# Optimization experiments

Measured on AMD Instinct MI355X. Metric: run time of the kernel, lower is better.

The kernel has to match this reference:

```python
import jax, jax.numpy as jnp
import numpy as np

B, N, C = 8, 4096, 512
H = W = 64           # N = H * W, dimensionality == 2
SHIFT = 4            # shift_size
WS = 8               # window_size
R = 4                # mlp_ratio
EPS = 1e-6


def setup_inputs() -> dict:
    key = jax.random.key(0)
    ks = jax.random.split(key, 3)
    return {
        "inputs": jax.random.normal(ks[0], (B, N, C), dtype=jnp.float32),
        # second_norm (LayerNormalization) params
        "ln_gamma": jnp.ones((C,), jnp.float32),
        "ln_beta": jnp.zeros((C,), jnp.float32),
        # MLP params: Dense(C*R) -> gelu -> Dense(C)
        "W1": jax.random.normal(ks[1], (C, C * R), dtype=jnp.float32) * 0.02,
        "b1": jnp.zeros((C * R,), jnp.float32),
        "W2": jax.random.normal(ks[2], (C * R, C), dtype=jnp.float32) * 0.02,
        "b2": jnp.zeros((C,), jnp.float32),
    }


def _layer_norm(x, gamma, beta):
    mu = jnp.mean(x, axis=-1, keepdims=True)
    var = jnp.mean(jnp.square(x - mu), axis=-1, keepdims=True)
    return (x - mu) * jax.lax.rsqrt(var + EPS) * gamma + beta


def reference(inputs, ln_gamma, ln_beta, W1, b1, W2, b2):
    # NOTE: faithful to the provided call(): first_norm and attention are
    # never invoked (`normed = x`, `self_att = windowed`), so the window
    # partition + reverse is an exact identity round-trip of the shifted grid.
    grid = inputs.reshape(B, H, W, C)
    shifted = jnp.roll(grid, (-SHIFT, -SHIFT), axis=(1, 2))  # SwinCyclicShifter

    # window partition: [B, nH, nW, WS, WS, C] windows of WSxWS patches
    nh = H // WS
    win = shifted.reshape(B, nh, WS, nh, WS, C).transpose(0, 1, 3, 2, 4, 5)
    # (identity "attention" on [B*nH*nW, WS*WS, C]) then window reverse
    unwin = win.transpose(0, 1, 3, 2, 4, 5).reshape(B, N, C)

    x = unwin + inputs                       # residual add
    normed = _layer_norm(x, ln_gamma, ln_beta)
    h = jax.nn.gelu(normed @ W1 + b1)        # [B, N, 4C]
    mlp_out = h @ W2 + b2                    # [B, N, C]
    return mlp_out + x
```

## Files before the change

### kernel.cpp

```cpp
#include <hip/hip_runtime.h>
#include <hip/hip_bf16.h>
#include <cstdint>
#include <cstddef>


typedef short bf16x8 __attribute__((ext_vector_type(8)));
typedef float f32x4 __attribute__((ext_vector_type(4)));

#define GLOBAL_AS(p) ((__attribute__((address_space(1))) void*)(uintptr_t)(p))
#define LDS_AS(p)    ((__attribute__((address_space(3))) void*)(p))

static __device__ __forceinline__ ushort f2bf(float f) {
    uint32_t u = __float_as_uint(f);
    uint32_t r = (u + 0x7FFFu + ((u >> 16) & 1u)) >> 16;
    return (ushort)r;
}

static __device__ __forceinline__ float gelu_s(float v) {
    float v2 = v * v;
    float m = fmaf(0.07135481283f, v2, 1.5957691216f);
    float e = __expf(-v * m);
    return v * __builtin_amdgcn_rcpf(1.0f + e);
}

static __device__ __forceinline__ int rolled_row(int row) {
    int b = row >> 12, n = row & 4095;
    int h = n >> 6, wv = n & 63;
    int n2 = (((h + 4) & 63) << 6) | ((wv + 4) & 63);
    return (b << 12) | n2;
}

#define SBAR() do { __builtin_amdgcn_sched_barrier(0); \
                    __builtin_amdgcn_s_barrier(); \
                    __builtin_amdgcn_sched_barrier(0); } while (0)

__global__ __launch_bounds__(128)
void ln_kernel(const float* __restrict__ in, const float* __restrict__ gamma,
               const float* __restrict__ beta, ushort* __restrict__ normed) {
    const int row = blockIdx.x;
    const int t = threadIdx.x;
    const int row2 = rolled_row(row);

    const float4* p0 = (const float4*)(in + (size_t)row * 512);
    const float4* p1 = (const float4*)(in + (size_t)row2 * 512);
    float4 a = p0[t], c = p1[t];
    float x0 = a.x + c.x, x1 = a.y + c.y, x2 = a.z + c.z, x3 = a.w + c.w;

    float s = x0 + x1 + x2 + x3;
    float sq = x0 * x0 + x1 * x1 + x2 * x2 + x3 * x3;
#pragma unroll
    for (int o = 32; o > 0; o >>= 1) {
        s += __shfl_xor(s, o);
        sq += __shfl_xor(sq, o);
    }
    __shared__ float red[4];
    if ((t & 63) == 0) { red[(t >> 6) * 2] = s; red[(t >> 6) * 2 + 1] = sq; }
    __syncthreads();
    s = red[0] + red[2];
    sq = red[1] + red[3];
    float mu = s * (1.0f / 512.0f);
    float var = sq * (1.0f / 512.0f) - mu * mu;
    float rs = rsqrtf(var + 1e-6f);

    float4 g = ((const float4*)gamma)[t];
    float4 be = ((const float4*)beta)[t];
    ushort4 o4;
    o4.x = f2bf((x0 - mu) * rs * g.x + be.x);
    o4.y = f2bf((x1 - mu) * rs * g.y + be.y);
    o4.z = f2bf((x2 - mu) * rs * g.z + be.z);
    o4.w = f2bf((x3 - mu) * rs * g.w + be.w);
    ((ushort4*)(normed + (size_t)row * 512))[t] = o4;
}

template <int PERM>
__global__ __launch_bounds__(256)
void transpose_cast(const float* __restrict__ src, ushort* __restrict__ dst,
                    int R, int Ccols) {
    __shared__ float tile[32][33];
    const int bx = blockIdx.x * 32;
    const int by = blockIdx.y * 32;
    const int tx = threadIdx.x, ty = threadIdx.y;
#pragma unroll
    for (int i = 0; i < 32; i += 8)
        tile[ty + i][tx] = src[(size_t)(by + ty + i) * Ccols + bx + tx];
    __syncthreads();
    int k = by + tx;
    int kd = PERM ? ((k & ~63) | ((k & 15) << 2) | ((k >> 4) & 3)) : k;
#pragma unroll
    for (int i = 0; i < 32; i += 8)
        dst[(size_t)(bx + ty + i) * R + kd] = f2bf(tile[tx][ty + i]);
}

__global__ __launch_bounds__(256)
void mlp_gemm1(const ushort* __restrict__ A, const ushort* __restrict__ Bt,
               const float* __restrict__ bias, ushort* __restrict__ outH) {
    constexpr int K = 512, N = 2048, BK = 32;
    __shared__ ushort Asm[128 * BK];
    __shared__ ushort Bsm[128 * BK];

    const int t = threadIdx.x;
    const int w = t >> 6, l = t & 63;
    const int wr = w >> 1, wc = w & 1;
    const int brow = blockIdx.y * 128;
    const int bcol = blockIdx.x * 128;

    f32x4 acc[4][4] = {};

    const int arow = t >> 2;
    const int acol = (t & 3) * 8;
    const size_t aBase = (size_t)(brow + arow) * K + acol;
    const size_t bBase = (size_t)(bcol + arow) * K + acol;
    char* ldsA = (char*)Asm + w * 1024;
    char* ldsB = (char*)Bsm + w * 1024;

    const int kb = (l >> 4) * 8;
    const int rA = l & 15;

    for (int k0 = 0; k0 < K; k0 += BK) {
        __builtin_amdgcn_global_load_lds(GLOBAL_AS(A + aBase + k0), LDS_AS(ldsA), 16, 0, 0);
        __builtin_amdgcn_global_load_lds(GLOBAL_AS(A + aBase + (size_t)64 * K + k0), LDS_AS(ldsA + 4096), 16, 0, 0);
        __builtin_amdgcn_global_load_lds(GLOBAL_AS(Bt + bBase + k0), LDS_AS(ldsB), 16, 0, 0);
        __builtin_amdgcn_global_load_lds(GLOBAL_AS(Bt + bBase + (size_t)64 * K + k0), LDS_AS(ldsB + 4096), 16, 0, 0);
        __syncthreads();

        bf16x8 aF[4], bF[4];
#pragma unroll
        for (int i = 0; i < 4; ++i)
            aF[i] = *(const bf16x8*)&Asm[(wr * 64 + i * 16 + rA) * BK + kb];
#pragma unroll
        for (int j = 0; j < 4; ++j)
            bF[j] = *(const bf16x8*)&Bsm[(wc * 64 + j * 16 + rA) * BK + kb];

#pragma unroll
        for (int i = 0; i < 4; ++i)
#pragma unroll
            for (int j = 0; j < 4; ++j)
                acc[i][j] = __builtin_amdgcn_mfma_f32_16x16x32_bf16(aF[i], bF[j], acc[i][j], 0, 0, 0);
        __syncthreads();
    }

    const int cm = (l >> 4) << 2;
    const int cn = l & 15;
    float bvv[4];
#pragma unroll
    for (int j = 0; j < 4; ++j)
        bvv[j] = bias[bcol + wc * 64 + j * 16 + cn];
    const int ecol = bcol + wc * 64 + (cn << 2);
#pragma unroll
    for (int i = 0; i < 4; ++i) {
#pragma unroll
        for (int r = 0; r < 4; ++r) {
            const int row = brow + wr * 64 + i * 16 + cm + r;
            float f0 = gelu_s(acc[i][0][r] + bvv[0]);
            float f1 = gelu_s(acc[i][1][r] + bvv[1]);
            float f2 = gelu_s(acc[i][2][r] + bvv[2]);
            float f3 = gelu_s(acc[i][3][r] + bvv[3]);
            uint32_t lo, hi;
            asm("v_cvt_pk_bf16_f32 %0, %1, %2" : "=v"(lo) : "v"(f0), "v"(f1));
            asm("v_cvt_pk_bf16_f32 %0, %1, %2" : "=v"(hi) : "v"(f2), "v"(f3));
            uint2 pv; pv.x = lo; pv.y = hi;
            *(uint2*)(outH + (size_t)row * N + ecol) = pv;
        }
    }
}

__global__ __launch_bounds__(512, 2)
void mlp_gemm2(const ushort* __restrict__ A, const ushort* __restrict__ Bt,
               const float* __restrict__ bias, const float* __restrict__ resid,
               float* __restrict__ outF) {
    constexpr int KT = 2048, TT = 32, N = 512;
    __shared__ __align__(16) char sm[131072];
    const int t = threadIdx.x;
    const int w = t >> 6, l = t & 63;
    const int wr = w >> 2, wc = w & 3;

    const int nwg = gridDim.x;
    const int bid = blockIdx.x;
    const int swz = (bid & 7) * (nwg >> 3) + (bid >> 3);
    const int cb = swz & 1;
    const int rgrp = swz >> 1;
    const int brow0 = rgrp * 256;
    const int bcol = cb << 8;

    const int kksw = (((t & 3) ^ ((t >> 4) & 3)) << 3);
    const size_t aTh = (size_t)(t >> 2) * KT + kksw;
    const size_t bTh = (size_t)(bcol + (t >> 2)) * KT + kksw;
    const ushort* const aPanel = A + (size_t)brow0 * KT;
    char* const dA = (char*)sm + (w << 10);
    char* const dB = dA + 65536;

    const int xorv = ((l >> 2) & 3) << 4;
    const int preA = ((((wr << 7) + (l & 15)) << 6) + ((l >> 4) << 4)) ^ xorv;
    const int preB = 65536 + (((((wc << 6) + (l & 15)) << 6) + ((l >> 4) << 4)) ^ xorv);

    f32x4 acc[8][4] = {};
    bf16x8 aF[4], bF[4];

    auto issueA = [&](int T, int kh) {
        const int slot = ((T & 1) << 1) | kh;
        const ushort* s = aPanel + aTh + T * 64 + kh * 32;
        char* d = dA + (slot << 14);
        __builtin_amdgcn_global_load_lds(GLOBAL_AS(s), LDS_AS(d), 16, 0, 0);
        __builtin_amdgcn_global_load_lds(GLOBAL_AS(s + (size_t)128 * KT), LDS_AS(d + 8192), 16, 0, 0);
    };
    auto issueB = [&](int T, int kh) {
        const int slot = ((T & 1) << 1) | kh;
        const ushort* s = Bt + bTh + T * 64 + kh * 32;
        char* d = dB + (slot << 14);
        __builtin_amdgcn_global_load_lds(GLOBAL_AS(s), LDS_AS(d), 16, 0, 0);
        __builtin_amdgcn_global_load_lds(GLOBAL_AS(s + (size_t)128 * KT), LDS_AS(d + 8192), 16, 0, 0);
    };
    auto rdA = [&](int slot, int mb) {
        const char* p = (const char*)sm + (slot << 14) + preA + (mb << 12);
        aF[0] = *(const bf16x8*)(p);
        aF[1] = *(const bf16x8*)(p + 1024);
        aF[2] = *(const bf16x8*)(p + 2048);
        aF[3] = *(const bf16x8*)(p + 3072);
    };
    auto rdB = [&](int slot) {
        const char* p = (const char*)sm + (slot << 14) + preB;
        bF[0] = *(const bf16x8*)(p);
        bF[1] = *(const bf16x8*)(p + 1024);
        bF[2] = *(const bf16x8*)(p + 2048);
        bF[3] = *(const bf16x8*)(p + 3072);
    };
    auto mfma16 = [&](int mb) {
        __builtin_amdgcn_s_setprio(1);
#pragma unroll
        for (int mf = 0; mf < 4; ++mf)
#pragma unroll
            for (int nf = 0; nf < 4; ++nf)
                acc[mb * 4 + mf][nf] = __builtin_amdgcn_mfma_f32_16x16x32_bf16(
                    aF[mf], bF[nf], acc[mb * 4 + mf][nf], 0, 0, 0);
        __builtin_amdgcn_s_setprio(0);
    };

    float bv[4];
#pragma unroll
    for (int nf = 0; nf < 4; ++nf)
        bv[nf] = bias[bcol + (wc << 6) + nf * 16 + (l & 15)];

    issueA(0, 0); issueB(0, 0);
    issueA(0, 1); issueB(0, 1);
    issueA(1, 0); issueB(1, 0);
    issueA(1, 1);
    __builtin_amdgcn_sched_barrier(0);
    asm volatile("s_waitcnt vmcnt(6)" ::: "memory");
    SBAR();

#pragma unroll 1
    for (int T = 0; T < TT; ++T) {
        const int s0 = (T & 1) << 1;
        rdA(s0, 0); rdB(s0);
        SBAR();
        if (T + 1 < TT) issueB(T + 1, 1);
        mfma16(0);
        SBAR();
        rdA(s0, 1);
        SBAR();
        if (T + 2 < TT) issueA(T + 2, 0);
        mfma16(1);
        SBAR();
        rdA(s0 + 1, 0); rdB(s0 + 1);
        SBAR();
        if (T + 2 < TT) issueB(T + 2, 0);
        mfma16(0);
        SBAR();
        rdA(s0 + 1, 1);
        SBAR();
        if (T + 2 < TT) issueA(T + 2, 1);
        mfma16(1);
        __builtin_amdgcn_sched_barrier(0);
        if (T < TT - 2)       { asm volatile("s_waitcnt vmcnt(6)" ::: "memory"); }
        else if (T == TT - 2) { asm volatile("s_waitcnt vmcnt(0)" ::: "memory"); }
        SBAR();
    }

    const int rbase = brow0 + (wr << 7) + ((l >> 4) << 2);
    const int cbase = bcol + (wc << 6) + (l & 15);
#pragma unroll
    for (int mf = 0; mf < 8; ++mf) {
#pragma unroll
        for (int r = 0; r < 4; ++r) {
            const int row = rbase + mf * 16 + r;
            const float* x0 = resid + (size_t)row * 512;
            const float* x1 = resid + (size_t)rolled_row(row) * 512;
#pragma unroll
            for (int nf = 0; nf < 4; ++nf) {
                const int col = cbase + nf * 16;
                outF[(size_t)row * N + col] =
                    acc[mf][nf][r] + bv[nf] + x0[col] + x1[col];
            }
        }
    }
}

extern "C" void kernel_launch(void* const* d_in, const int* in_sizes, int n_in,
                              void* d_out, int out_size, void* d_ws, size_t ws_size,
                              hipStream_t stream) {
    const float* in = (const float*)d_in[0];
    const float* ln_g = (const float*)d_in[1];
    const float* ln_b = (const float*)d_in[2];
    const float* W1 = (const float*)d_in[3];
    const float* b1 = (const float*)d_in[4];
    const float* W2 = (const float*)d_in[5];
    const float* b2 = (const float*)d_in[6];
    float* out = (float*)d_out;

    char* ws = (char*)d_ws;
    ushort* normed = (ushort*)ws;
    ushort* hbuf   = (ushort*)(ws + (size_t)32 * 1024 * 1024);
    ushort* W1T    = (ushort*)(ws + (size_t)160 * 1024 * 1024);
    ushort* W2T    = (ushort*)(ws + (size_t)162 * 1024 * 1024);

    const int M = 32768;
    const int C = 512, C4 = 2048;

    ln_kernel<<<M, 128, 0, stream>>>(in, ln_g, ln_b, normed);
    transpose_cast<0><<<dim3(C4 / 32, C / 32), dim3(32, 8), 0, stream>>>(W1, W1T, C, C4);
    transpose_cast<1><<<dim3(C / 32, C4 / 32), dim3(32, 8), 0, stream>>>(W2, W2T, C4, C);

    mlp_gemm1<<<dim3(C4 / 128, M / 128), 256, 0, stream>>>(normed, W1T, b1, hbuf);
    mlp_gemm2<<<dim3(256), 512, 0, stream>>>(hbuf, W2T, b2, in, out);
}
```

Before: 220.5 us.

## Swizzle GEMM1 LDS, remap blocks per XCD, stage GEMM2 epilogue through LDS

GEMM1 now uses a 1D grid whose block index is remapped so that consecutive blocks on each XCD share A row tiles, which should improve L2 reuse. Its LDS layout gets an XOR swizzle on the k-chunk to avoid bank conflicts on fragment reads. GEMM2's epilogue writes accumulators to LDS and then does coalesced float4 stores with vectorized bias and residual loads, replacing scattered scalar stores. The staging adds two block-wide barriers per half and reuses shared memory.

```diff
diff --git a/kernel.cpp b/kernel.cpp
--- a/kernel.cpp
+++ b/kernel.cpp
@@ -101,20 +101,23 @@
     const int t = threadIdx.x;
     const int w = t >> 6, l = t & 63;
     const int wr = w >> 1, wc = w & 1;
-    const int brow = blockIdx.y * 128;
-    const int bcol = blockIdx.x * 128;
+
+    const int bid = blockIdx.x;
+    const int xcd = bid & 7, idx = bid >> 3;
+    const int brow = ((xcd << 5) + (idx >> 4)) << 7;
+    const int bcol = (idx & 15) << 7;
 
     f32x4 acc[4][4] = {};
 
     const int arow = t >> 2;
-    const int acol = (t & 3) * 8;
-    const size_t aBase = (size_t)(brow + arow) * K + acol;
-    const size_t bBase = (size_t)(bcol + arow) * K + acol;
+    const int kchunk = (((t & 3) ^ ((t >> 4) & 3)) << 3);
+    const size_t aBase = (size_t)(brow + arow) * K + kchunk;
+    const size_t bBase = (size_t)(bcol + arow) * K + kchunk;
     char* ldsA = (char*)Asm + w * 1024;
     char* ldsB = (char*)Bsm + w * 1024;
 
-    const int kb = (l >> 4) * 8;
-    const int rA = l & 15;
+    const int slotA = (((l >> 4) ^ ((l >> 2) & 3)) << 4);
+    const int rA = l & 63 & 15;
 
     for (int k0 = 0; k0 < K; k0 += BK) {
         __builtin_amdgcn_global_load_lds(GLOBAL_AS(A + aBase + k0), LDS_AS(ldsA), 16, 0, 0);
@@ -126,10 +129,10 @@
         bf16x8 aF[4], bF[4];
 #pragma unroll
         for (int i = 0; i < 4; ++i)
-            aF[i] = *(const bf16x8*)&Asm[(wr * 64 + i * 16 + rA) * BK + kb];
+            aF[i] = *(const bf16x8*)((const char*)Asm + (wr * 64 + i * 16 + rA) * 64 + slotA);
 #pragma unroll
         for (int j = 0; j < 4; ++j)
-            bF[j] = *(const bf16x8*)&Bsm[(wc * 64 + j * 16 + rA) * BK + kb];
+            bF[j] = *(const bf16x8*)((const char*)Bsm + (wc * 64 + j * 16 + rA) * 64 + slotA);
 
 #pragma unroll
         for (int i = 0; i < 4; ++i)
@@ -235,11 +238,6 @@
         __builtin_amdgcn_s_setprio(0);
     };
 
-    float bv[4];
-#pragma unroll
-    for (int nf = 0; nf < 4; ++nf)
-        bv[nf] = bias[bcol + (wc << 6) + nf * 16 + (l & 15)];
-
     issueA(0, 0); issueB(0, 0);
     issueA(0, 1); issueB(0, 1);
     issueA(1, 0); issueB(1, 0);
@@ -276,22 +274,35 @@
         SBAR();
     }
 
-    const int rbase = brow0 + (wr << 7) + ((l >> 4) << 2);
-    const int cbase = bcol + (wc << 6) + (l & 15);
-#pragma unroll
-    for (int mf = 0; mf < 8; ++mf) {
-#pragma unroll
-        for (int r = 0; r < 4; ++r) {
-            const int row = rbase + mf * 16 + r;
-            const float* x0 = resid + (size_t)row * 512;
-            const float* x1 = resid + (size_t)rolled_row(row) * 512;
-#pragma unroll
-            for (int nf = 0; nf < 4; ++nf) {
-                const int col = cbase + nf * 16;
-                outF[(size_t)row * N + col] =
-                    acc[mf][nf][r] + bv[nf] + x0[col] + x1[col];
-            }
+#pragma unroll
+    for (int h2 = 0; h2 < 2; ++h2) {
+        if (wr == h2) {
+#pragma unroll
+            for (int mf = 0; mf < 8; ++mf)
+#pragma unroll
+                for (int nf = 0; nf < 4; ++nf)
+#pragma unroll
+                    for (int r = 0; r < 4; ++r) {
+                        int rl = mf * 16 + ((l >> 4) << 2) + r;
+                        int col = (wc << 6) + nf * 16 + (l & 15);
+                        *(float*)(sm + rl * 1024 + col * 4) = acc[mf][nf][r];
+                    }
         }
+        __syncthreads();
+#pragma unroll
+        for (int k = 0; k < 16; ++k) {
+            int c = t + (k << 9);
+            int row = c >> 6, c4 = c & 63;
+            f32x4 v = *(const f32x4*)(sm + ((size_t)c << 4));
+            int R = brow0 + (h2 << 7) + row;
+            int col0 = bcol + (c4 << 2);
+            f32x4 bb = *(const f32x4*)(bias + col0);
+            f32x4 x0 = *(const f32x4*)(resid + (size_t)R * 512 + col0);
+            f32x4 x1 = *(const f32x4*)(resid + (size_t)rolled_row(R) * 512 + col0);
+            v = v + bb + x0 + x1;
+            *(f32x4*)(outF + (size_t)R * N + col0) = v;
+        }
+        __syncthreads();
     }
 }
 
@@ -320,6 +331,6 @@
     transpose_cast<0><<<dim3(C4 / 32, C / 32), dim3(32, 8), 0, stream>>>(W1, W1T, C, C4);
     transpose_cast<1><<<dim3(C / 32, C4 / 32), dim3(32, 8), 0, stream>>>(W2, W2T, C4, C);
 
-    mlp_gemm1<<<dim3(C4 / 128, M / 128), 256, 0, stream>>>(normed, W1T, b1, hbuf);
+    mlp_gemm1<<<dim3(4096), 256, 0, stream>>>(normed, W1T, b1, hbuf);
     mlp_gemm2<<<dim3(256), 512, 0, stream>>>(hbuf, W2T, b2, in, out);
 }
```

After: 217.8 us. Within noise of the previous version (-1.2%).
